# Performance work log

Measured on AMD Instinct MI355X. Metric: run time of the kernel, lower is better.

Reference implementation:

```python
import jax, jax.numpy as jnp
from jax import lax
import numpy as np

B, S, H, L = 128, 256, 768, 24


def setup_inputs() -> dict:
    key = jax.random.key(0)
    k_tf, k_len, k_w, k_tr, k_st, k_en = jax.random.split(key, 6)
    token_features = jax.random.normal(k_tf, (B, S, H), dtype=jnp.float32)
    # contiguous valid lengths in [3, S] (>=3 so that stripping CLS/SEP leaves >=1 token)
    lengths = jax.random.randint(k_len, (B,), 3, S + 1)
    pos = jnp.arange(S)
    input_mask = (pos[None, :] < lengths[:, None]).astype(jnp.int32)
    true_label_mask = (pos[None, :] < (lengths - 2)[:, None]).astype(jnp.int32)
    W = jax.random.normal(k_w, (H, L), dtype=jnp.float32) * 0.02
    b = jnp.zeros((L,), dtype=jnp.float32)
    transitions = jax.random.normal(k_tr, (L, L), dtype=jnp.float32) * 0.1
    start_trans = jax.random.normal(k_st, (L,), dtype=jnp.float32) * 0.1
    end_trans = jax.random.normal(k_en, (L,), dtype=jnp.float32) * 0.1
    return {
        "token_features": token_features,
        "input_mask": input_mask,
        "true_label_mask": true_label_mask,
        "W": W,
        "b": b,
        "transitions": transitions,
        "start_trans": start_trans,
        "end_trans": end_trans,
    }


def _compact(x, mask):
    """Vectorized version of the torch per-token copy loop: for each row,
    gather valid tokens (mask==1) preserving order, drop the first and last
    valid token (CLS/SEP), left-pack into a zero tensor."""
    # stable argsort puts valid positions first, in order
    order = jnp.argsort(1 - mask.astype(jnp.int32), axis=1)  # [B,S]
    gathered = jnp.take_along_axis(x, order[:, :, None], axis=1)  # [B,S,H]
    # drop first valid token (shift left by 1), pad a zero row at the end
    shifted = jnp.concatenate([gathered[:, 1:], jnp.zeros_like(gathered[:, :1])], axis=1)
    n_valid = mask.sum(axis=1)  # [B]
    keep = jnp.arange(x.shape[1])[None, :] < (n_valid[:, None] - 2)  # also drops last (SEP)
    return jnp.where(keep[:, :, None], shifted, 0.0)


def _viterbi(emissions, mask, transitions, start_trans, end_trans):
    """Masked Viterbi decode. emissions [B,S,L], mask [B,S] bool."""
    Bn, Sn, Ln = emissions.shape
    lbl = jnp.arange(Ln)
    score0 = start_trans[None, :] + emissions[:, 0]  # [B,L]

    def step(score, xs):
        em_t, m_t = xs  # [B,L], [B]
        cand = score[:, :, None] + transitions[None]  # [B,prev,curr]
        best = cand.max(axis=1) + em_t
        bp = cand.argmax(axis=1)  # [B,L] best prev tag per curr tag
        new_score = jnp.where(m_t[:, None], best, score)
        bp = jnp.where(m_t[:, None], bp, lbl[None, :])  # identity backpointer on pad
        return new_score, bp

    ems = jnp.swapaxes(emissions[:, 1:], 0, 1)  # [S-1,B,L]
    ms = jnp.swapaxes(mask[:, 1:], 0, 1)  # [S-1,B]
    final, bps = lax.scan(step, score0, (ems, ms))
    final = final + end_trans[None, :]
    best_score = final.max(axis=1)  # [B]
    last_tag = final.argmax(axis=1)  # [B]

    def back(tag, bp):  # tag: tag at time t; bp: bp_t -> tag at t-1
        prev = jnp.take_along_axis(bp, tag[:, None], axis=1)[:, 0]
        return prev, tag

    tag0, tags_rest = lax.scan(back, last_tag, bps, reverse=True)  # tags_rest [S-1,B]
    path = jnp.concatenate([tag0[:, None], jnp.swapaxes(tags_rest, 0, 1)], axis=1)  # [B,S]
    return best_score, path


def reference(token_features, input_mask, true_label_mask, W, b, transitions, start_trans, end_trans):
    mask = input_mask.astype(bool)
    wv = _compact(token_features, mask)  # dropout is identity at inference
    emissions = jax.nn.sigmoid(wv @ W + b)  # [B,S,L]
    _, path = _viterbi(emissions, true_label_mask != 0, transitions, start_trans, end_trans)
    return path
```

## Files before the change

### kernel.cpp

```cpp
#include <hip/hip_runtime.h>
#include <hip/hip_bf16.h>
#include <math.h>

#define NB 128
#define NS 256
#define NH 768
#define NL 24

__global__ __launch_bounds__(256) void ner_emis(
    const float* __restrict__ tf, const int* __restrict__ tlm,
    const float* __restrict__ W, const float* __restrict__ bias,
    float* __restrict__ E)
{
    const int b    = blockIdx.x >> 2;
    const int tile = (blockIdx.x & 3) << 6;
    const int tid  = threadIdx.x;
    if (tlm[b*NS + tile] == 0) return;

    __shared__ float As[64*65];
    __shared__ float P2[2*64*25];

    const int lane = tid & 63;
    const int w    = __builtin_amdgcn_readfirstlane(tid >> 6);
    const int koff = w << 4;

    float acc[NL];
    #pragma unroll
    for (int l = 0; l < NL; ++l) acc[l] = 0.f;

    const float* tfb = tf + (size_t)(b*NS)*NH;

    for (int kc0 = 0; kc0 < NH; kc0 += 64) {
        #pragma unroll
        for (int i = 0; i < 4; ++i) {
            int idx  = tid + (i << 8);
            int row  = idx >> 4;
            int c4   = idx & 15;
            int trow = tile + row + 1;
            if (trow > 255) trow = 255;
            float4 v = *(const float4*)(tfb + (size_t)trow*NH + kc0 + (c4 << 2));
            float* dst = As + row*65 + (c4 << 2);
            dst[0] = v.x; dst[1] = v.y; dst[2] = v.z; dst[3] = v.w;
        }
        __syncthreads();

        #pragma unroll
        for (int k = 0; k < 16; ++k) {
            float a = As[lane*65 + koff + k];
            const float* wr = W + (size_t)(kc0 + koff + k)*NL;
            #pragma unroll
            for (int l = 0; l < NL; ++l) acc[l] = fmaf(a, wr[l], acc[l]);
        }
        __syncthreads();
    }

    if (w & 1) {
        float* p = P2 + ((w >> 1)*64 + lane)*25;
        #pragma unroll
        for (int l = 0; l < NL; ++l) p[l] = acc[l];
    }
    __syncthreads();
    if (!(w & 1)) {
        const float* p = P2 + ((w >> 1)*64 + lane)*25;
        #pragma unroll
        for (int l = 0; l < NL; ++l) acc[l] += p[l];
    }
    __syncthreads();
    if (!(w & 1)) {
        float* p = P2 + ((w >> 1)*64 + lane)*25;
        #pragma unroll
        for (int l = 0; l < NL; ++l) p[l] = acc[l];
    }
    __syncthreads();

    const int* tm = tlm + b*NS + tile;
    float* Eb = E + (size_t)(b*NS + tile)*NL;
    #pragma unroll
    for (int j = 0; j < 6; ++j) {
        int idx = tid + (j << 8);
        int tok = idx / NL, l = idx % NL;
        if (tm[tok]) {
            float s = P2[(0*64 + tok)*25 + l] + P2[(1*64 + tok)*25 + l];
            float x = s + bias[l];
            Eb[tok*NL + l] = 1.0f/(1.0f + expf(-x));
        }
    }
}

__global__ __launch_bounds__(256) void ner_viterbi(
    const float* __restrict__ E, const int* __restrict__ tlm,
    const float* __restrict__ trans, const float* __restrict__ st,
    const float* __restrict__ en, int* __restrict__ out)
{
    const int tid = threadIdx.x;
    const int b   = blockIdx.x;
    const int bS  = b*NS;

    __shared__ float Esh[NS*NL];
    __shared__ float scl[NS*NL];
    __shared__ float Tt[NL*NL];
    __shared__ float fin[NL];
    __shared__ unsigned char tr_s[NL][NS];
    __shared__ int chosen[12];
    __shared__ int nsh, ltag;

    {
        const float4* src = (const float4*)(E + (size_t)bS*NL);
        float4* dst = (float4*)Esh;
        #pragma unroll
        for (int j = 0; j < 6; ++j) dst[tid + (j << 8)] = src[tid + (j << 8)];
    }
    for (int i = tid; i < NL*NL; i += 256) {
        int c = i / NL, p = i % NL;
        Tt[i] = trans[p*NL + c];
    }
    if (tid < 64) {
        int a = tlm[bS+tid] + tlm[bS+tid+64] + tlm[bS+tid+128] + tlm[bS+tid+192];
        #pragma unroll
        for (int off = 32; off > 0; off >>= 1) a += __shfl_down(a, off, 64);
        if (tid == 0) nsh = a;
    }
    __syncthreads();
    const int n = nsh;

    if (tid < 64) {
        const int c = tid % 24;
        float Tc[24];
        #pragma unroll
        for (int p = 0; p < 24; ++p) Tc[p] = trans[p*NL + c];

        auto rl = [](float v, int p) {
            return __int_as_float(__builtin_amdgcn_readlane(__float_as_int(v), p));
        };

        float sv = st[c] + Esh[c];
        scl[c] = sv;
        float scr[24];
        #pragma unroll
        for (int p = 0; p < 24; ++p) scr[p] = rl(sv, p);

        auto step = [&](int t, float em) {
            float cand[24];
            #pragma unroll
            for (int p = 0; p < 24; ++p) cand[p] = scr[p] + Tc[p];
            float m0 = fmaxf(fmaxf(cand[0],  cand[1]),  cand[2]);
            float m1 = fmaxf(fmaxf(cand[3],  cand[4]),  cand[5]);
            float m2 = fmaxf(fmaxf(cand[6],  cand[7]),  cand[8]);
            float m3 = fmaxf(fmaxf(cand[9],  cand[10]), cand[11]);
            float m4 = fmaxf(fmaxf(cand[12], cand[13]), cand[14]);
            float m5 = fmaxf(fmaxf(cand[15], cand[16]), cand[17]);
            float m6 = fmaxf(fmaxf(cand[18], cand[19]), cand[20]);
            float m7 = fmaxf(fmaxf(cand[21], cand[22]), cand[23]);
            float q0 = fmaxf(fmaxf(m0, m1), m2);
            float q1 = fmaxf(fmaxf(m3, m4), m5);
            float q2 = fmaxf(m6, m7);
            float best = fmaxf(fmaxf(q0, q1), q2);
            sv = best + em;
            scl[t*NL + c] = sv;
            #pragma unroll
            for (int p = 0; p < 24; ++p) scr[p] = rl(sv, p);
        };

        int t = 1;
        for (; t + 8 <= n; t += 8) {
            float em[8];
            const float* eb = Esh + t*NL + c;
            #pragma unroll
            for (int j = 0; j < 8; ++j) em[j] = eb[j*NL];
            #pragma unroll
            for (int j = 0; j < 8; ++j) step(t + j, em[j]);
        }
        for (; t < n; ++t) step(t, Esh[t*NL + c]);
        fin[c] = sv + en[c];
    }
    __syncthreads();

    if (tid == 0) {
        float bv = fin[0]; int bt = 0;
        #pragma unroll
        for (int cc = 1; cc < 24; ++cc) { if (fin[cc] > bv) { bv = fin[cc]; bt = cc; } }
        ltag = bt;
    }
    __syncthreads();

    const int K = (n > 1) ? (n - 1 + 9) / 10 : 1;
    if (n > 1 && tid < 240) {
        const int w = tid / 24 + 1, h = tid % 24;
        int tlo = (w-1)*K; if (tlo > n-1) tlo = n-1;
        int thi = w*K;     if (thi > n-1) thi = n-1;
        int cur = h;
        for (int t = thi; t > tlo; --t) {
            const float4* sp = (const float4*)(scl + (t-1)*NL);
            const float4* up = (const float4*)(Tt  + cur*NL);
            float cand[24];
            #pragma unroll
            for (int i = 0; i < 6; ++i) {
                float4 s = sp[i], u = up[i];
                cand[4*i+0] = s.x + u.x;
                cand[4*i+1] = s.y + u.y;
                cand[4*i+2] = s.z + u.z;
                cand[4*i+3] = s.w + u.w;
            }
            float best = cand[0]; int arg = 0;
            #pragma unroll
            for (int p = 1; p < 24; ++p) { if (cand[p] > best) { best = cand[p]; arg = p; } }
            tr_s[h][t-1] = (unsigned char)arg;
            cur = arg;
        }
    }
    __syncthreads();

    if (tid == 0) {
        int cur = ltag;
        for (int w = 10; w >= 1; --w) {
            chosen[w] = cur;
            int tlo = (w-1)*K; if (tlo > n-1) tlo = n-1;
            int thi = w*K;     if (thi > n-1) thi = n-1;
            if (thi > tlo) cur = tr_s[cur][tlo];
        }
    }
    __syncthreads();

    {
        const int t = tid;
        int tag;
        if (t >= n-1) tag = ltag;
        else { int w = t / K + 1; tag = tr_s[chosen[w]][t]; }
        out[bS + t] = tag;
    }
}

extern "C" void kernel_launch(void* const* d_in, const int* in_sizes, int n_in,
                              void* d_out, int out_size, void* d_ws, size_t ws_size,
                              hipStream_t stream) {
    const float* tf    = (const float*)d_in[0];
    const int*   tlm   = (const int*)  d_in[2];
    const float* W     = (const float*)d_in[3];
    const float* bias  = (const float*)d_in[4];
    const float* trans = (const float*)d_in[5];
    const float* st    = (const float*)d_in[6];
    const float* en    = (const float*)d_in[7];
    float* E = (float*)d_ws;

    ner_emis<<<dim3(NB*4), dim3(256), 0, stream>>>(tf, tlm, W, bias, E);
    ner_viterbi<<<dim3(NB), dim3(256), 0, stream>>>(E, tlm, trans, st, en, (int*)d_out);
}
```

Baseline: 226.4 us.

## Retile emission GEMM to 32-token blocks with LDS-staged W and split-K

The emission kernel now uses 32-token tiles, which doubles the grid, and stages each 64-row chunk of W in shared memory instead of reading it from global memory per FMA. Each thread computes two tokens over a 4-wide k slice, with rotated k order to reduce bank conflicts, and the 16 k-partials are reduced through LDS in two stages. The aim is more parallelism, less redundant global W traffic and higher FMA-per-load reuse. In exchange it adds more reduction work and doubles the accumulator registers.

```diff
diff --git a/kernel.cpp b/kernel.cpp
--- a/kernel.cpp
+++ b/kernel.cpp
@@ -6,83 +6,112 @@
 #define NS 256
 #define NH 768
 #define NL 24
+#define ASTR 68
 
 __global__ __launch_bounds__(256) void ner_emis(
     const float* __restrict__ tf, const int* __restrict__ tlm,
     const float* __restrict__ W, const float* __restrict__ bias,
     float* __restrict__ E)
 {
-    const int b    = blockIdx.x >> 2;
-    const int tile = (blockIdx.x & 3) << 6;
+    const int b    = blockIdx.x >> 3;
+    const int tile = (blockIdx.x & 7) << 5;
     const int tid  = threadIdx.x;
     if (tlm[b*NS + tile] == 0) return;
 
-    __shared__ float As[64*65];
-    __shared__ float P2[2*64*25];
-
-    const int lane = tid & 63;
-    const int w    = __builtin_amdgcn_readfirstlane(tid >> 6);
-    const int koff = w << 4;
-
-    float acc[NL];
+    __shared__ float lds[8*32*25];
+    float* As = lds;
+    float* Ws = lds + 32*ASTR;
+    float* Pr = lds;
+
+    const int tok  = tid & 15;
+    const int ksub = tid >> 4;
+    const int kk   = ksub << 2;
+    const int rot  = ksub & 3;
+
+    float acc0[NL], acc1[NL];
     #pragma unroll
-    for (int l = 0; l < NL; ++l) acc[l] = 0.f;
+    for (int l = 0; l < NL; ++l) { acc0[l] = 0.f; acc1[l] = 0.f; }
 
     const float* tfb = tf + (size_t)(b*NS)*NH;
 
     for (int kc0 = 0; kc0 < NH; kc0 += 64) {
         #pragma unroll
-        for (int i = 0; i < 4; ++i) {
+        for (int i = 0; i < 2; ++i) {
             int idx  = tid + (i << 8);
             int row  = idx >> 4;
             int c4   = idx & 15;
             int trow = tile + row + 1;
             if (trow > 255) trow = 255;
             float4 v = *(const float4*)(tfb + (size_t)trow*NH + kc0 + (c4 << 2));
-            float* dst = As + row*65 + (c4 << 2);
+            float* dst = As + row*ASTR + (c4 << 2);
             dst[0] = v.x; dst[1] = v.y; dst[2] = v.z; dst[3] = v.w;
         }
+        {
+            const float4* wsrc = (const float4*)(W + (size_t)kc0*NL);
+            float4* wdst = (float4*)Ws;
+            for (int i = tid; i < 384; i += 256) wdst[i] = wsrc[i];
+        }
         __syncthreads();
 
-        #pragma unroll
-        for (int k = 0; k < 16; ++k) {
-            float a = As[lane*65 + koff + k];
-            const float* wr = W + (size_t)(kc0 + koff + k)*NL;
-            #pragma unroll
-            for (int l = 0; l < NL; ++l) acc[l] = fmaf(a, wr[l], acc[l]);
+        const float* A0 = As + tok*ASTR + kk;
+        const float* A1 = A0 + 16*ASTR;
+        const float* Wr = Ws + kk*NL;
+        #pragma unroll
+        for (int s = 0; s < 4; ++s) {
+            const int j = (s + rot) & 3;
+            float a0 = A0[j];
+            float a1 = A1[j];
+            const float4* w4 = (const float4*)(Wr + j*NL);
+            float wv[NL];
+            #pragma unroll
+            for (int i = 0; i < 6; ++i) {
+                float4 w = w4[i];
+                wv[4*i+0] = w.x; wv[4*i+1] = w.y; wv[4*i+2] = w.z; wv[4*i+3] = w.w;
+            }
+            #pragma unroll
+            for (int l = 0; l < NL; ++l) {
+                acc0[l] = fmaf(a0, wv[l], acc0[l]);
+                acc1[l] = fmaf(a1, wv[l], acc1[l]);
+            }
         }
         __syncthreads();
     }
 
-    if (w & 1) {
-        float* p = P2 + ((w >> 1)*64 + lane)*25;
-        #pragma unroll
-        for (int l = 0; l < NL; ++l) p[l] = acc[l];
-    }
-    __syncthreads();
-    if (!(w & 1)) {
-        const float* p = P2 + ((w >> 1)*64 + lane)*25;
-        #pragma unroll
-        for (int l = 0; l < NL; ++l) acc[l] += p[l];
-    }
-    __syncthreads();
-    if (!(w & 1)) {
-        float* p = P2 + ((w >> 1)*64 + lane)*25;
-        #pragma unroll
-        for (int l = 0; l < NL; ++l) p[l] = acc[l];
+    if (ksub >= 8) {
+        float* p = Pr + ((ksub-8)*32 + tok)*25;
+        float* q = p + 16*25;
+        #pragma unroll
+        for (int l = 0; l < NL; ++l) { p[l] = acc0[l]; q[l] = acc1[l]; }
+    }
+    __syncthreads();
+    if (ksub < 8) {
+        const float* p = Pr + (ksub*32 + tok)*25;
+        const float* q = p + 16*25;
+        #pragma unroll
+        for (int l = 0; l < NL; ++l) { acc0[l] += p[l]; acc1[l] += q[l]; }
+    }
+    __syncthreads();
+    if (ksub < 8) {
+        float* p = Pr + (ksub*32 + tok)*25;
+        float* q = p + 16*25;
+        #pragma unroll
+        for (int l = 0; l < NL; ++l) { p[l] = acc0[l]; q[l] = acc1[l]; }
     }
     __syncthreads();
 
     const int* tm = tlm + b*NS + tile;
     float* Eb = E + (size_t)(b*NS + tile)*NL;
     #pragma unroll
-    for (int j = 0; j < 6; ++j) {
-        int idx = tid + (j << 8);
-        int tok = idx / NL, l = idx % NL;
-        if (tm[tok]) {
-            float s = P2[(0*64 + tok)*25 + l] + P2[(1*64 + tok)*25 + l];
+    for (int i = 0; i < 3; ++i) {
+        int o = tid + (i << 8);
+        int t = o / NL, l = o % NL;
+        if (tm[t]) {
+            float s = 0.f;
+            #pragma unroll
+            for (int ks = 0; ks < 8; ++ks)
+                s += Pr[(ks*32 + t)*25 + l];
             float x = s + bias[l];
-            Eb[tok*NL + l] = 1.0f/(1.0f + expf(-x));
+            Eb[t*NL + l] = 1.0f/(1.0f + expf(-x));
         }
     }
 }
@@ -242,6 +271,6 @@
     const float* en    = (const float*)d_in[7];
     float* E = (float*)d_ws;
 
-    ner_emis<<<dim3(NB*4), dim3(256), 0, stream>>>(tf, tlm, W, bias, E);
+    ner_emis<<<dim3(NB*8), dim3(256), 0, stream>>>(tf, tlm, W, bias, E);
     ner_viterbi<<<dim3(NB), dim3(256), 0, stream>>>(E, tlm, trans, st, en, (int*)d_out);
 }
```

New measurement: 207.5 us. -8.4%, faster.
